# Kernel optimization log

Hardware: AMD Instinct MI355X
Metric: run time of the kernel (lower is better)

## Reference

```python
import jax, jax.numpy as jnp
import numpy as np

EPS = 1e-12  # torch F.normalize default eps

def _l2norm(x):
    n = jnp.sqrt(jnp.sum(x * x, axis=-1, keepdims=True))
    return x / jnp.maximum(n, EPS)

def setup_inputs() -> dict:
    key = jax.random.key(0)
    k1, k2, k3 = jax.random.split(key, 3)
    N, S, D = 65536, 2048, 512
    return {
        "query": jax.random.normal(k1, (N, D), dtype=jnp.float32),
        "keys": jax.random.normal(k2, (S, D), dtype=jnp.float32),
        "values": jax.random.normal(k3, (S, D), dtype=jnp.float32),
    }

def reference(query, keys, values):
    q = _l2norm(query)            # [N, D]
    k = _l2norm(keys)             # [S, D]
    scores = jnp.einsum('nd,sd->ns', q, k)   # [N, S] cosine scores
    attn = jax.nn.softmax(scores, axis=-1)   # [N, S]
    return jnp.einsum('ns,sd->nd', attn, values)  # [N, D]
```

## Files before the change

### kernel.cpp

```cpp
#include <hip/hip_runtime.h>
#include <hip/hip_bf16.h>

typedef __attribute__((ext_vector_type(8))) short short8;
typedef __attribute__((ext_vector_type(4))) float f32x4;
typedef __attribute__((ext_vector_type(2))) unsigned int u32x2;

constexpr int D_DIM = 512;
constexpr int S_DIM = 2048;

static __device__ __forceinline__ unsigned short f2bf(float f) {
  __hip_bfloat16 h = __float2bfloat16(f);
  return *reinterpret_cast<unsigned short*>(&h);
}

#define GLP(p) ((const __attribute__((address_space(1))) unsigned int*)(p))
#define LDP(p) ((__attribute__((address_space(3))) unsigned int*)(p))

static __device__ __forceinline__ void blockbar() {
  asm volatile("" ::: "memory");
  __builtin_amdgcn_s_barrier();
  asm volatile("" ::: "memory");
}

__global__ void k_norm(const float* __restrict__ K, ushort* __restrict__ Kn) {
  const int row = blockIdx.x * 4 + (threadIdx.x >> 6);
  const int l   = threadIdx.x & 63;
  const float* src = K + (size_t)row * D_DIM + l * 8;
  float4 v0 = *(const float4*)(src);
  float4 v1 = *(const float4*)(src + 4);
  float ss = v0.x*v0.x + v0.y*v0.y + v0.z*v0.z + v0.w*v0.w
           + v1.x*v1.x + v1.y*v1.y + v1.z*v1.z + v1.w*v1.w;
  #pragma unroll
  for (int off = 1; off < 64; off <<= 1) ss += __shfl_xor(ss, off, 64);
  const float sc = 1.0f / fmaxf(sqrtf(ss), 1e-12f);
  float f[8] = {v0.x,v0.y,v0.z,v0.w,v1.x,v1.y,v1.z,v1.w};
  unsigned uu[4];
  #pragma unroll
  for (int i = 0; i < 4; ++i)
    uu[i] = (unsigned)f2bf(f[2*i]*sc) | ((unsigned)f2bf(f[2*i+1]*sc) << 16);
  *(uint4*)(Kn + (size_t)row * D_DIM + l*8) = make_uint4(uu[0],uu[1],uu[2],uu[3]);
}

__global__ void k_transpose_v(const float* __restrict__ V, ushort* __restrict__ Vt) {
  __shared__ float tile[64][65];
  const int s0 = blockIdx.x * 64;
  const int d0 = blockIdx.y * 64;
  const int tj = threadIdx.x & 63;
  const int ti = threadIdx.x >> 6;
  #pragma unroll
  for (int k = 0; k < 16; ++k) {
    int s = ti + 4*k;
    tile[s][tj] = V[(size_t)(s0+s) * D_DIM + d0 + tj];
  }
  __syncthreads();
  #pragma unroll
  for (int k = 0; k < 16; ++k) {
    int d = ti + 4*k;
    Vt[(size_t)(d0+d) * S_DIM + s0 + tj] = f2bf(tile[tj][d]);
  }
}

template <int EPI>
__global__ __launch_bounds__(512, 2) void gemm_bt(
    const ushort* __restrict__ A, const ushort* __restrict__ B,
    int aStride, int bStride,
    int NT,
    ushort* __restrict__ Pout, float* __restrict__ Oout,
    int ldC)
{
  __shared__ ushort lds[2][4][8192];
  char* ldsb = (char*)&lds[0][0][0];

  const int tid = threadIdx.x;
  const int w   = tid >> 6;
  const int l   = tid & 63;
  const int lhi = l >> 4;
  const int llo = l & 15;
  const int wm  = w >> 2;
  const int wn  = w & 3;
  const size_t m0 = (size_t)blockIdx.x * 256;
  const size_t n0 = (size_t)blockIdx.y * 256;

  const char* Ab = (const char*)A;
  const char* Bb = (const char*)B;

  const int srow = tid >> 3;
  const int scb  = (tid & 7) * 16;
  auto stage = [&](int buf, int slot, int t) {
    const char* src; int stride; size_t r0;
    if (slot < 2) { src = Ab; stride = aStride; r0 = m0 + (size_t)slot * 128; }
    else          { src = Bb; stride = bStride; r0 = n0 + (size_t)(slot - 2) * 128; }
    char* lbase = ldsb + ((buf*4 + slot) * 16384) + w * 1024;
    {
      const int row = srow;
      const char* g = src + (r0 + row) * (size_t)stride + t*128 + (scb ^ ((row & 7) << 4));
      __builtin_amdgcn_global_load_lds(GLP(g), LDP(lbase), 16, 0, 0);
    }
    {
      const int row = srow + 64;
      const char* g = src + (r0 + row) * (size_t)stride + t*128 + (scb ^ ((row & 7) << 4));
      __builtin_amdgcn_global_load_lds(GLP(g), LDP(lbase + 8192), 16, 0, 0);
    }
  };

  const unsigned swz = (unsigned)((l & 7) << 4);
  short8 ar[4][2], br01[2][2], br23[2][2];
  f32x4 acc[8][4] = {};
  f32x4 acc_rs[8] = {};
  short8 ones;
  #pragma unroll
  for (int i = 0; i < 8; ++i) ones[i] = (short)0x3F80;

  const char* aBase0 = ldsb + wm * 16384;
  const char* bBase0 = ldsb + (2 + (wn >> 1)) * 16384;
  const unsigned bRow0 = (unsigned)((wn & 1) * 64);

  auto readA = [&](int buf, int rfB) {
    const char* base = aBase0 + buf * 65536;
    #pragma unroll
    for (int rf = 0; rf < 4; ++rf)
      #pragma unroll
      for (int kk = 0; kk < 2; ++kk) {
        unsigned off = (unsigned)(((rfB + rf) * 16 + llo) * 128)
                     + (((unsigned)(kk*64 + lhi*16)) ^ swz);
        ar[rf][kk] = *(const short8*)(base + off);
      }
  };
  auto readB = [&](int buf, int cfB, short8 (&br)[2][2]) {
    const char* base = bBase0 + buf * 65536;
    #pragma unroll
    for (int c = 0; c < 2; ++c)
      #pragma unroll
      for (int kk = 0; kk < 2; ++kk) {
        unsigned off = (unsigned)((bRow0 + (cfB + c) * 16 + llo) * 128)
                     + (((unsigned)(kk*64 + lhi*16)) ^ swz);
        br[c][kk] = *(const short8*)(base + off);
      }
  };
  auto quad = [&](int rfB, int cfB, short8 (&br)[2][2]) {
    __builtin_amdgcn_s_setprio(1);
    #pragma unroll
    for (int kk = 0; kk < 2; ++kk) {
      #pragma unroll
      for (int rf = 0; rf < 4; ++rf) {
        #pragma unroll
        for (int c = 0; c < 2; ++c)
          acc[rfB+rf][cfB+c] = __builtin_amdgcn_mfma_f32_16x16x32_bf16(
              ar[rf][kk], br[c][kk], acc[rfB+rf][cfB+c], 0, 0, 0);
        if (EPI == 1 && cfB == 0)
          acc_rs[rfB+rf] = __builtin_amdgcn_mfma_f32_16x16x32_bf16(
              ar[rf][kk], ones, acc_rs[rfB+rf], 0, 0, 0);
      }
    }
    __builtin_amdgcn_s_setprio(0);
  };

  stage(0, 2, 0); stage(0, 0, 0); stage(0, 1, 0); stage(0, 3, 0);
  stage(1, 2, 1); stage(1, 0, 1);

  for (int t = 0; t < NT; ++t) {
    const int cur = t & 1, nxt = cur ^ 1;
    if (t + 1 < NT) asm volatile("s_waitcnt vmcnt(4)" ::: "memory");
    else            asm volatile("s_waitcnt vmcnt(0)" ::: "memory");
    blockbar();
    readA(cur, 0);
    readB(cur, 0, br01);
    if (t + 1 < NT) stage(nxt, 1, t + 1);
    quad(0, 0, br01);
    blockbar();
    readB(cur, 2, br23);
    if (t + 1 < NT) stage(nxt, 3, t + 1);
    quad(0, 2, br23);
    blockbar();
    readA(cur, 4);
    if (t + 2 < NT) stage(cur, 2, t + 2);
    quad(4, 2, br23);
    blockbar();
    if (t + 2 < NT) stage(cur, 0, t + 2);
    quad(4, 0, br01);
  }

  if (EPI == 0) {
    #pragma unroll
    for (int rf = 0; rf < 8; ++rf) {
      float e[4][4];
      #pragma unroll
      for (int cf = 0; cf < 4; ++cf)
        #pragma unroll
        for (int j = 0; j < 4; ++j)
          e[cf][j] = __expf(acc[rf][cf][j]);
      #pragma unroll
      for (int j = 0; j < 4; ++j) {
        const size_t m = m0 + wm*128 + rf*16 + lhi*4 + j;
        #pragma unroll
        for (int cf = 0; cf < 4; ++cf) {
          const size_t n = n0 + wn*64 + cf*16 + llo;
          Pout[m * (size_t)ldC + n] = f2bf(e[cf][j]);
        }
      }
    }
  } else {
    #pragma unroll
    for (int rf = 0; rf < 8; ++rf)
      #pragma unroll
      for (int j = 0; j < 4; ++j) {
        const size_t m = m0 + wm*128 + rf*16 + lhi*4 + j;
        const float inv = 1.0f / acc_rs[rf][j];
        #pragma unroll
        for (int cf = 0; cf < 4; ++cf) {
          const size_t n = n0 + wn*64 + cf*16 + llo;
          Oout[m * (size_t)ldC + n] = acc[rf][cf][j] * inv;
        }
      }
  }
}

constexpr int BMf = 64, BHf = 256, NHf = S_DIM / BHf, NWf = 8;
constexpr int PBUFf = BMf * BHf * 2;

__global__ __launch_bounds__(512, 2) void attn_fused(
    const float* __restrict__ Q, const ushort* __restrict__ Kn,
    const ushort* __restrict__ Vt, float* __restrict__ out)
{
  __shared__ ushort q_s[BMf * D_DIM];
  __shared__ ushort p_s[2 * BMf * BHf];
  __shared__ float  rs_lds[NWf * BMf];
  __shared__ float  rs_tot[BMf];
  char* qb = (char*)q_s;
  char* pb = (char*)p_s;
  const int tid = threadIdx.x;
  const int w   = tid >> 6;
  const int l   = tid & 63;
  const int lhi = l >> 4;
  const int llo = l & 15;
  const size_t q0 = (size_t)blockIdx.x * BMf;
  {
    const int row = tid >> 3;
    const int c   = tid & 7;
    const unsigned swzr = (unsigned)((row & 7) << 4);
    const float4* src = (const float4*)(Q + (q0 + row) * D_DIM);
    float4 t[16];
    float ss = 0.f;
    #pragma unroll
    for (int i = 0; i < 16; ++i) {
      t[i] = src[c + i*8];
      ss += t[i].x*t[i].x + t[i].y*t[i].y + t[i].z*t[i].z + t[i].w*t[i].w;
    }
    ss += __shfl_xor(ss, 1, 64);
    ss += __shfl_xor(ss, 2, 64);
    ss += __shfl_xor(ss, 4, 64);
    const float sc = 1.0f / fmaxf(sqrtf(ss), 1e-12f);
    #pragma unroll
    for (int i = 0; i < 16; ++i) {
      u32x2 pv;
      pv[0] = (unsigned)f2bf(t[i].x*sc) | ((unsigned)f2bf(t[i].y*sc) << 16);
      pv[1] = (unsigned)f2bf(t[i].z*sc) | ((unsigned)f2bf(t[i].w*sc) << 16);
      unsigned byte = (unsigned)(row*1024) + (((unsigned)(c*8 + i*64)) ^ swzr);
      *(u32x2*)(qb + byte) = pv;
    }
  }
  __syncthreads();
  f32x4 o[4][4] = {};
  float rs_acc[4] = {0.f, 0.f, 0.f, 0.f};
  const unsigned swz = (unsigned)((l & 7) << 4);
  unsigned rowbQ[4], rowbP[4];
  #pragma unroll
  for (int qf = 0; qf < 4; ++qf) {
    rowbQ[qf] = (unsigned)((qf*16 + llo) * 1024);
    rowbP[qf] = (unsigned)((qf*16 + llo) * 512);
  }
  auto do_qkt = [&](int h, f32x4 (&sacc)[2][4]) {
    const short8* kp[2];
    #pragma unroll
    for (int kf = 0; kf < 2; ++kf)
      kp[kf] = (const short8*)(Kn + (size_t)(h*BHf + w*32 + kf*16 + llo) * D_DIM + lhi*8);
    __builtin_amdgcn_s_setprio(1);
    #pragma unroll
    for (int ks = 0; ks < 16; ++ks) {
      const unsigned off = ((unsigned)(ks*64 + lhi*16)) ^ swz;
      short8 a[2], b[4];
      #pragma unroll
      for (int kf = 0; kf < 2; ++kf) a[kf] = kp[kf][ks*4];
      #pragma unroll
      for (int qf = 0; qf < 4; ++qf)
        b[qf] = *(const short8*)(qb + (rowbQ[qf] + off));
      #pragma unroll
      for (int kf = 0; kf < 2; ++kf)
        #pragma unroll
        for (int qf = 0; qf < 4; ++qf)
          sacc[kf][qf] = __builtin_amdgcn_mfma_f32_16x16x32_bf16(a[kf], b[qf], sacc[kf][qf], 0, 0, 0);
    }
    __builtin_amdgcn_s_setprio(0);
  };
  auto do_exp = [&](f32x4 (&sacc)[2][4], u32x2 (&pk)[2][4]) {
    #pragma unroll
    for (int kf = 0; kf < 2; ++kf)
      #pragma unroll
      for (int qf = 0; qf < 4; ++qf) {
        float p0 = __expf(sacc[kf][qf][0]);
        float p1 = __expf(sacc[kf][qf][1]);
        float p2 = __expf(sacc[kf][qf][2]);
        float p3 = __expf(sacc[kf][qf][3]);
        rs_acc[qf] += (p0 + p1) + (p2 + p3);
        pk[kf][qf][0] = (unsigned)f2bf(p0) | ((unsigned)f2bf(p1) << 16);
        pk[kf][qf][1] = (unsigned)f2bf(p2) | ((unsigned)f2bf(p3) << 16);
      }
  };
  auto do_pwrite = [&](u32x2 (&pk)[2][4], char* buf) {
    #pragma unroll
    for (int kf = 0; kf < 2; ++kf)
      #pragma unroll
      for (int qf = 0; qf < 4; ++qf) {
        unsigned lin = (unsigned)(w*64 + kf*32 + lhi*8);
        *(u32x2*)(buf + rowbP[qf] + (lin ^ swz)) = pk[kf][qf];
      }
  };
  auto do_pv = [&](int h, const char* buf) {
    const short8* vp[4];
    #pragma unroll
    for (int df = 0; df < 4; ++df)
      vp[df] = (const short8*)(Vt + (size_t)(w*64 + df*16 + llo) * S_DIM + h*BHf + lhi*8);
    __builtin_amdgcn_s_setprio(1);
    #pragma unroll
    for (int ks = 0; ks < 8; ++ks) {
      const unsigned off = ((unsigned)(ks*64 + lhi*16)) ^ swz;
      short8 a[4], b[4];
      #pragma unroll
      for (int qf = 0; qf < 4; ++qf)
        a[qf] = *(const short8*)(buf + (rowbP[qf] + off));
      #pragma unroll
      for (int df = 0; df < 4; ++df) b[df] = vp[df][ks*4];
      #pragma unroll
      for (int qf = 0; qf < 4; ++qf)
        #pragma unroll
        for (int df = 0; df < 4; ++df)
          o[qf][df] = __builtin_amdgcn_mfma_f32_16x16x32_bf16(a[qf], b[df], o[qf][df], 0, 0, 0);
    }
    __builtin_amdgcn_s_setprio(0);
  };
  {
    f32x4 sacc[2][4] = {};
    do_qkt(0, sacc);
    u32x2 pk[2][4];
    do_exp(sacc, pk);
    do_pwrite(pk, pb + 0);
  }
  __syncthreads();
  for (int i = 0; i < NHf - 1; ++i) {
    f32x4 sacc[2][4] = {};
    do_qkt(i + 1, sacc);
    u32x2 pk[2][4];
    do_exp(sacc, pk);
    do_pv(i, pb + (i & 1) * PBUFf);
    do_pwrite(pk, pb + ((i + 1) & 1) * PBUFf);
    __syncthreads();
  }
  do_pv(NHf - 1, pb + ((NHf - 1) & 1) * PBUFf);
  #pragma unroll
  for (int qf = 0; qf < 4; ++qf) {
    float v = rs_acc[qf];
    v += __shfl_xor(v, 16, 64);
    v += __shfl_xor(v, 32, 64);
    if (l < 16) rs_lds[w*BMf + qf*16 + llo] = v;
  }
  __syncthreads();
  if (tid < BMf) {
    float tot = 0.f;
    #pragma unroll
    for (int ww = 0; ww < NWf; ++ww) tot += rs_lds[ww*BMf + tid];
    rs_tot[tid] = tot;
  }
  __syncthreads();
  #pragma unroll
  for (int qf = 0; qf < 4; ++qf)
    #pragma unroll
    for (int r = 0; r < 4; ++r) {
      const int query = qf*16 + lhi*4 + r;
      const float inv = 1.0f / rs_tot[query];
      #pragma unroll
      for (int df = 0; df < 4; ++df) {
        const int dim = w*64 + df*16 + llo;
        out[(q0 + query) * D_DIM + dim] = o[qf][df][r] * inv;
      }
    }
}

extern "C" void kernel_launch(void* const* d_in, const int* in_sizes, int n_in,
                              void* d_out, int out_size, void* d_ws, size_t ws_size,
                              hipStream_t stream) {
  const float* Q = (const float*)d_in[0];
  const float* K = (const float*)d_in[1];
  const float* V = (const float*)d_in[2];
  float* out = (float*)d_out;
  const int N = in_sizes[0] / D_DIM;

  ushort* Kn = (ushort*)d_ws;
  ushort* Vt = Kn + (size_t)S_DIM * D_DIM;
  char*   rest = (char*)(Vt + (size_t)D_DIM * S_DIM);
  const size_t base_bytes = (size_t)S_DIM * D_DIM * 2 * 2;
  const size_t avail = ws_size > base_bytes ? ws_size - base_bytes : 0;

  const size_t perRow = (size_t)D_DIM*2 + (size_t)S_DIM*2;
  int chunk = 0;
  const int cand[4] = {32768, 16384, 8192, 4096};
  for (int i = 0; i < 4; ++i)
    if ((size_t)cand[i] * perRow <= avail && (N % cand[i]) == 0) { chunk = cand[i]; break; }

  k_norm<<<S_DIM/4, 256, 0, stream>>>(K, Kn);
  k_transpose_v<<<dim3(S_DIM/64, D_DIM/64), 256, 0, stream>>>(V, Vt);

  if (chunk == 0) {
    attn_fused<<<N/BMf, 512, 0, stream>>>(Q, Kn, Vt, out);
    return;
  }

  ushort* Qn = (ushort*)rest;
  ushort* P  = Qn + (size_t)chunk * D_DIM;

  for (int c = 0; c < N; c += chunk) {
    k_norm<<<chunk/4, 256, 0, stream>>>(Q + (size_t)c * D_DIM, Qn);
    gemm_bt<0><<<dim3(chunk/256, S_DIM/256), 512, 0, stream>>>(
        Qn, Kn, D_DIM*2, D_DIM*2, D_DIM/64, P, nullptr, S_DIM);
    gemm_bt<1><<<dim3(chunk/256, D_DIM/256), 512, 0, stream>>>(
        P, Vt, S_DIM*2, S_DIM*2, S_DIM/64, nullptr,
        out + (size_t)c * D_DIM, D_DIM);
  }
}
```

Measured before the change: 352.9 us.

## Add single-buffered 128x256 QK^T GEMM kernel with higher occupancy

Replaces the first GEMM (normalized Q times K^T with exp epilogue) with a new kernel. It uses a 128x256 block tile, a single-buffered 48KB LDS stage instead of the double-buffered 4-slot layout, and launch bounds allowing four blocks per CU. The aim is to rely on occupancy rather than in-block double buffering to hide load latency. In exchange the kernel waits on global loads each k-step with no prefetch overlap, and the smaller M tile means more B reloads.

```diff
diff --git a/kernel.cpp b/kernel.cpp
--- a/kernel.cpp
+++ b/kernel.cpp
@@ -57,6 +57,101 @@
   for (int k = 0; k < 16; ++k) {
     int d = ti + 4*k;
     Vt[(size_t)(d0+d) * S_DIM + s0 + tj] = f2bf(tile[tj][d]);
+  }
+}
+
+__global__ __launch_bounds__(512, 4) void gemm1_sb(
+    const ushort* __restrict__ A, const ushort* __restrict__ B,
+    int aStride, int bStride,
+    int NT,
+    ushort* __restrict__ Pout, int ldC)
+{
+  __shared__ ushort lds[3][8192];
+  char* ldsb = (char*)&lds[0][0];
+
+  const int tid = threadIdx.x;
+  const int w   = tid >> 6;
+  const int l   = tid & 63;
+  const int lhi = l >> 4;
+  const int llo = l & 15;
+  const int wm  = w >> 2;
+  const int wn  = w & 3;
+  const size_t m0 = (size_t)blockIdx.x * 128;
+  const size_t n0 = (size_t)blockIdx.y * 256;
+
+  const int srow = tid >> 3;
+  const int scb  = (tid & 7) * 16;
+  const unsigned sw = (unsigned)(scb ^ ((srow & 7) << 4));
+  const char* gp[3][2];
+  #pragma unroll
+  for (int slot = 0; slot < 3; ++slot) {
+    const char* src; int stride; size_t r0;
+    if (slot == 0) { src = (const char*)A; stride = aStride; r0 = m0; }
+    else           { src = (const char*)B; stride = bStride; r0 = n0 + (size_t)(slot - 1) * 128; }
+    gp[slot][0] = src + (r0 + srow) * (size_t)stride + sw;
+    gp[slot][1] = src + (r0 + srow + 64) * (size_t)stride + sw;
+  }
+  auto stage = [&](int slot, int t) {
+    char* lbase = ldsb + slot * 16384 + w * 1024;
+    const int toff = t * 128;
+    __builtin_amdgcn_global_load_lds(GLP(gp[slot][0] + toff), LDP(lbase), 16, 0, 0);
+    __builtin_amdgcn_global_load_lds(GLP(gp[slot][1] + toff), LDP(lbase + 8192), 16, 0, 0);
+  };
+
+  const unsigned swz = (unsigned)((l & 7) << 4);
+  f32x4 acc[4][4] = {};
+
+  const unsigned aRow0 = (unsigned)(wm * 64);
+  const int bSlot = 1 + (wn >> 1);
+  const unsigned bRow0 = (unsigned)((wn & 1) * 64);
+  const char* aBase = ldsb;
+  const char* bBase = ldsb + bSlot * 16384;
+
+  stage(0, 0); stage(1, 0); stage(2, 0);
+
+  for (int t = 0; t < NT; ++t) {
+    asm volatile("s_waitcnt vmcnt(0)" ::: "memory");
+    blockbar();
+    #pragma unroll
+    for (int kk = 0; kk < 2; ++kk) {
+      short8 ar[4], br[4];
+      const unsigned koff = ((unsigned)(kk*64 + lhi*16)) ^ swz;
+      #pragma unroll
+      for (int rf = 0; rf < 4; ++rf)
+        ar[rf] = *(const short8*)(aBase + (aRow0 + rf*16 + llo) * 128 + koff);
+      #pragma unroll
+      for (int cf = 0; cf < 4; ++cf)
+        br[cf] = *(const short8*)(bBase + (bRow0 + cf*16 + llo) * 128 + koff);
+      __builtin_amdgcn_s_setprio(1);
+      #pragma unroll
+      for (int rf = 0; rf < 4; ++rf)
+        #pragma unroll
+        for (int cf = 0; cf < 4; ++cf)
+          acc[rf][cf] = __builtin_amdgcn_mfma_f32_16x16x32_bf16(
+              ar[rf], br[cf], acc[rf][cf], 0, 0, 0);
+      __builtin_amdgcn_s_setprio(0);
+    }
+    blockbar();
+    if (t + 1 < NT) { stage(0, t + 1); stage(1, t + 1); stage(2, t + 1); }
+  }
+
+  #pragma unroll
+  for (int rf = 0; rf < 4; ++rf) {
+    float e[4][4];
+    #pragma unroll
+    for (int cf = 0; cf < 4; ++cf)
+      #pragma unroll
+      for (int j = 0; j < 4; ++j)
+        e[cf][j] = __expf(acc[rf][cf][j]);
+    #pragma unroll
+    for (int j = 0; j < 4; ++j) {
+      const size_t m = m0 + wm*64 + rf*16 + lhi*4 + j;
+      #pragma unroll
+      for (int cf = 0; cf < 4; ++cf) {
+        const size_t n = n0 + wn*64 + cf*16 + llo;
+        Pout[m * (size_t)ldC + n] = f2bf(e[cf][j]);
+      }
+    }
   }
 }
 
@@ -419,8 +514,8 @@
 
   for (int c = 0; c < N; c += chunk) {
     k_norm<<<chunk/4, 256, 0, stream>>>(Q + (size_t)c * D_DIM, Qn);
-    gemm_bt<0><<<dim3(chunk/256, S_DIM/256), 512, 0, stream>>>(
-        Qn, Kn, D_DIM*2, D_DIM*2, D_DIM/64, P, nullptr, S_DIM);
+    gemm1_sb<<<dim3(chunk/128, S_DIM/256), 512, 0, stream>>>(
+        Qn, Kn, D_DIM*2, D_DIM*2, D_DIM/64, P, S_DIM);
     gemm_bt<1><<<dim3(chunk/256, D_DIM/256), 512, 0, stream>>>(
         P, Vt, S_DIM*2, S_DIM*2, S_DIM/64, nullptr,
         out + (size_t)c * D_DIM, D_DIM);
```

New measurement: 345.5 us. 1.02x faster.
